# Optimization experiments

Measured on AMD Instinct MI355X. Metric: run time of the kernel, lower is better.

## Reference

```python
import jax, jax.numpy as jnp
import numpy as np

IN_F = 64
EDGE_F = 64
B, N = 2, 512


def setup_inputs() -> dict:
    key = jax.random.key(0)
    ks = jax.random.split(key, 10)
    h = jax.random.normal(ks[0], (B, N, IN_F), dtype=jnp.float32)
    edge = jax.random.normal(ks[1], (B, N, N, EDGE_F), dtype=jnp.float32)
    adj = (jax.random.uniform(ks[2], (B, N, N)) < 0.5).astype(jnp.float32)
    lin_in = 2 * IN_F + EDGE_F
    s_lin = 1.0 / np.sqrt(lin_in)
    s_gru = 1.0 / np.sqrt(EDGE_F)
    W_lin = jax.random.uniform(ks[3], (EDGE_F, lin_in), minval=-s_lin, maxval=s_lin)
    b_lin = jax.random.uniform(ks[4], (EDGE_F,), minval=-s_lin, maxval=s_lin)
    w_ih = jax.random.uniform(ks[5], (3 * EDGE_F, EDGE_F), minval=-s_gru, maxval=s_gru)
    w_hh = jax.random.uniform(ks[6], (3 * EDGE_F, EDGE_F), minval=-s_gru, maxval=s_gru)
    b_ih = jax.random.uniform(ks[7], (3 * EDGE_F,), minval=-s_gru, maxval=s_gru)
    b_hh = jax.random.uniform(ks[8], (3 * EDGE_F,), minval=-s_gru, maxval=s_gru)
    return {"h": h, "edge": edge, "adj": adj, "W_lin": W_lin, "b_lin": b_lin,
            "w_ih": w_ih, "w_hh": w_hh, "b_ih": b_ih, "b_hh": b_hh}


def reference(h, edge, adj, W_lin, b_lin, w_ih, w_hh, b_ih, b_hh):
    F_ = h.shape[-1]
    E = edge.shape[-1]
    # Split the concat-linear: cat = [h1, edge, h2] where h1[b,i,j]=h[b,j], h2[b,i,j]=h[b,i].
    W1 = W_lin[:, :F_]            # cols acting on h1
    We = W_lin[:, F_:F_ + E]      # cols acting on edge
    W2 = W_lin[:, F_ + E:]        # cols acting on h2
    t1 = jnp.einsum('bjf,ef->bje', h, W1)[:, None, :, :]   # broadcast over i
    t2 = jnp.einsum('bif,ef->bie', h, W2)[:, :, None, :]   # broadcast over j
    te = jnp.einsum('bije,fe->bijf', edge, We)
    m = (t1 + te + t2 + b_lin) * adj[..., None]            # [b,N,N,E]
    # GRUCell: input = m, hidden = edge
    gi = jnp.einsum('bije,ge->bijg', m, w_ih) + b_ih        # [b,N,N,3E]
    gh = jnp.einsum('bije,ge->bijg', edge, w_hh) + b_hh
    i_r, i_z, i_n = jnp.split(gi, 3, axis=-1)
    h_r, h_z, h_n = jnp.split(gh, 3, axis=-1)
    r = jax.nn.sigmoid(i_r + h_r)
    z = jax.nn.sigmoid(i_z + h_z)
    n = jnp.tanh(i_n + r * h_n)
    new_h = (1.0 - z) * n + z * edge
    return jax.nn.silu(new_h)
```

## Files before the change

### kernel.cpp

```cpp
#include <hip/hip_runtime.h>
#include <hip/hip_bf16.h>

#define B_ 2
#define N_ 512
#define E_ 64
#define G_ 192
#define LIN_IN_ 192

typedef __attribute__((ext_vector_type(8))) short bf16x8;
typedef __attribute__((ext_vector_type(4))) float f32x4;

__device__ __forceinline__ unsigned short f2bf(float x) {
  unsigned u = __float_as_uint(x);
  unsigned r = (u + 0x7FFFu + ((u >> 16) & 1u)) >> 16;
  return (unsigned short)r;
}
__device__ __forceinline__ float sigm(float x) { return 1.f / (1.f + __expf(-x)); }
__device__ __forceinline__ float tanh_f(float x) {
  float e = __expf(-2.f * fabsf(x));
  return copysignf((1.f - e) / (1.f + e), x);
}
__device__ __forceinline__ bf16x8 pack8(const float* t) {
  union { bf16x8 v; __hip_bfloat16 h[8]; } u;
#pragma unroll
  for (int k = 0; k < 8; ++k) u.h[k] = __float2bfloat16(t[k]);
  return u.v;
}

__global__ __launch_bounds__(64) void prep1(const float* __restrict__ Wlin,
                                            const float* __restrict__ blin,
                                            const float* __restrict__ wih,
                                            const float* __restrict__ whh,
                                            unsigned short* __restrict__ Bt,
                                            float* __restrict__ V1,
                                            float* __restrict__ V2,
                                            float* __restrict__ ub) {
  int g = blockIdx.x;
  int f = threadIdx.x;
  if (g < G_) {
    const float* wr = wih + g * 64;
    float aw = 0.f, a1 = 0.f, a2 = 0.f;
#pragma unroll
    for (int e = 0; e < 64; ++e) {
      float wv = wr[e];
      a1 += wv * Wlin[e * LIN_IN_ + f];
      aw += wv * Wlin[e * LIN_IN_ + 64 + f];
      a2 += wv * Wlin[e * LIN_IN_ + 128 + f];
    }
    Bt[g * 64 + f] = f2bf(aw);
    V1[g * 64 + f] = a1;
    V2[g * 64 + f] = a2;
    if (f == 0) {
      float s = 0.f;
      for (int e = 0; e < 64; ++e) s += wr[e] * blin[e];
      ub[g] = s;
    }
  } else {
    int gh = g - G_;
    Bt[g * 64 + f] = f2bf(whh[gh * 64 + f]);
  }
}

__global__ __launch_bounds__(192) void prep2(const float* __restrict__ h,
                                             const float* __restrict__ V1,
                                             const float* __restrict__ V2,
                                             const float* __restrict__ ub,
                                             float* __restrict__ u1,
                                             float* __restrict__ u2p) {
  int row = blockIdx.x;
  int g = threadIdx.x;
  const float* hr = h + (size_t)row * 64;
  float a1 = 0.f, a2 = 0.f;
#pragma unroll
  for (int f = 0; f < 64; ++f) {
    float hv = hr[f];
    a1 += V1[g * 64 + f] * hv;
    a2 += V2[g * 64 + f] * hv;
  }
  u1[(size_t)row * G_ + g] = a1;
  u2p[(size_t)row * G_ + g] = a2 + ub[g];
}

__global__ __launch_bounds__(256, 3) void fusedT3(const float* __restrict__ edge,
                                                  const float* __restrict__ adj,
                                                  const unsigned short* __restrict__ BtW,
                                                  const float* __restrict__ u1,
                                                  const float* __restrict__ u2p,
                                                  const float* __restrict__ bih,
                                                  const float* __restrict__ bhh,
                                                  float* __restrict__ out) {
  __shared__ uint4 Bs4[3072];
  char* Bc = (char*)Bs4;
  int tid = threadIdx.x;
  const uint4* src = (const uint4*)BtW;
#pragma unroll
  for (int it = 0; it < 12; ++it) {
    int c = tid + it * 256;
    int row = c >> 3;
    *(uint4*)(Bc + row * 128 + (((c & 7) * 16) ^ ((row & 7) << 4))) = src[c];
  }
  __syncthreads();

  int lane = tid & 63, wave = tid >> 6;
  unsigned pbase = blockIdx.x * 128u + wave * 32u;
  int b = pbase >> 18;
  int iN = (pbase >> 9) & 511;
  int j0w = pbase & 511;
  int lr = lane & 15, lg = lane >> 4;

  bf16x8 efrag[2][2];
  float adjv[2];
#pragma unroll
  for (int np = 0; np < 2; ++np) {
    const float* er = edge + (size_t)(pbase + np * 16 + lr) * 64 + lg * 8;
    float tmp[8];
#pragma unroll
    for (int s = 0; s < 2; ++s) {
      *(float4*)tmp = *(const float4*)(er + s * 32);
      *(float4*)(tmp + 4) = *(const float4*)(er + s * 32 + 4);
      efrag[np][s] = pack8(tmp);
    }
    adjv[np] = adj[pbase + np * 16 + lr];
  }

  int addrE = (lr + 16 * (lg >> 1)) << 2;
  int addrO = addrE + 128;

  const float* u2r = u2p + ((size_t)(b * N_ + iN)) * G_;
  const float* u1b = u1 + ((size_t)(b * N_ + j0w)) * G_;

  f32x4 yo[2][4];

#pragma unroll
  for (int mg = 0; mg < 4; ++mg) {
    int e0 = mg * 16 + lg * 4;
    f32x4 acc[2][6];
    f32x4 zero = {0.f, 0.f, 0.f, 0.f};
#pragma unroll
    for (int np = 0; np < 2; ++np)
#pragma unroll
      for (int w = 0; w < 6; ++w) acc[np][w] = zero;

    const int tiles[6] = {mg, mg + 4, mg + 8, mg + 12, mg + 16, mg + 20};
#pragma unroll
    for (int s = 0; s < 2; ++s) {
      bf16x8 wf[6];
#pragma unroll
      for (int w = 0; w < 6; ++w) {
        int R = tiles[w] * 16 + lr;
        wf[w] = *(const bf16x8*)(Bc + R * 128 +
                                 ((s * 64 + lg * 16) ^ ((R & 7) << 4)));
      }
#pragma unroll
      for (int np = 0; np < 2; ++np)
#pragma unroll
        for (int w = 0; w < 6; ++w)
          acc[np][w] = __builtin_amdgcn_mfma_f32_16x16x32_bf16(
              wf[w], efrag[np][s], acc[np][w], 0, 0, 0);
    }

    f32x4 u2v0 = *(const f32x4*)(u2r + e0);
    f32x4 u2v1 = *(const f32x4*)(u2r + 64 + e0);
    f32x4 u2v2 = *(const f32x4*)(u2r + 128 + e0);
    f32x4 bc0 = *(const f32x4*)(bih + e0) + *(const f32x4*)(bhh + e0);
    f32x4 bc1 = *(const f32x4*)(bih + 64 + e0) + *(const f32x4*)(bhh + 64 + e0);
    f32x4 bi2 = *(const f32x4*)(bih + 128 + e0);
    f32x4 bh2 = *(const f32x4*)(bhh + 128 + e0);

#pragma unroll
    for (int np = 0; np < 2; ++np) {
      const float* u1r = u1b + (size_t)(np * 16 + lr) * G_;
      f32x4 u1v0 = *(const f32x4*)(u1r + e0);
      f32x4 u1v1 = *(const f32x4*)(u1r + 64 + e0);
      f32x4 u1v2 = *(const f32x4*)(u1r + 128 + e0);

      union { bf16x8 v; int d[4]; } ef;
      ef.v = efrag[np][mg >> 1];
      int addr = (mg & 1) ? addrO : addrE;
      int r0 = __builtin_amdgcn_ds_bpermute(addr, ef.d[0]);
      int r1 = __builtin_amdgcn_ds_bpermute(addr, ef.d[1]);
      int r2 = __builtin_amdgcn_ds_bpermute(addr, ef.d[2]);
      int r3 = __builtin_amdgcn_ds_bpermute(addr, ef.d[3]);
      bool hi = (lg & 1);
      unsigned w0 = (unsigned)(hi ? r2 : r0);
      unsigned w1 = (unsigned)(hi ? r3 : r1);
      float eva[4];
      eva[0] = __uint_as_float(w0 << 16);
      eva[1] = __uint_as_float(w0 & 0xffff0000u);
      eva[2] = __uint_as_float(w1 << 16);
      eva[3] = __uint_as_float(w1 & 0xffff0000u);

      float a = adjv[np];
      f32x4 yv;
#pragma unroll
      for (int reg = 0; reg < 4; ++reg) {
        float s1 = a * (acc[np][0][reg] + u1v0[reg] + u2v0[reg]) + bc0[reg] +
                   acc[np][3][reg];
        float s2 = a * (acc[np][1][reg] + u1v1[reg] + u2v1[reg]) + bc1[reg] +
                   acc[np][4][reg];
        float gin = a * (acc[np][2][reg] + u1v2[reg] + u2v2[reg]) + bi2[reg];
        float ghn = acc[np][5][reg] + bh2[reg];
        float r = sigm(s1);
        float z = sigm(s2);
        float n = tanh_f(gin + r * ghn);
        float y = (1.f - z) * n + z * eva[reg];
        yv[reg] = y * sigm(y);
      }
      yo[np][mg] = yv;
    }
  }

#pragma unroll
  for (int np = 0; np < 2; ++np) {
    size_t P = pbase + np * 16 + lr;
    float* op = out + P * 64 + lg * 4;
#pragma unroll
    for (int mg = 0; mg < 4; ++mg)
      *(f32x4*)(op + mg * 16) = yo[np][mg];
  }
}

__global__ __launch_bounds__(64) void mkernelF(const float* __restrict__ edge,
                                               const float* __restrict__ adj,
                                               const float* __restrict__ Wlin,
                                               const float* __restrict__ blin,
                                               const float* __restrict__ h,
                                               float* __restrict__ mout) {
  size_t p = (size_t)blockIdx.x * 64 + threadIdx.x;
  int b = (int)(p >> 18), i = (int)((p >> 9) & 511), j = (int)(p & 511);
  float ed[E_], hj[E_], hi[E_];
  const float4* ep = (const float4*)(edge + p * E_);
  const float4* hjp = (const float4*)(h + ((size_t)(b * N_ + j)) * E_);
  const float4* hip = (const float4*)(h + ((size_t)(b * N_ + i)) * E_);
#pragma unroll
  for (int k = 0; k < E_ / 4; ++k) {
    float4 v = ep[k];
    ed[4 * k] = v.x; ed[4 * k + 1] = v.y; ed[4 * k + 2] = v.z; ed[4 * k + 3] = v.w;
    float4 a = hjp[k];
    hj[4 * k] = a.x; hj[4 * k + 1] = a.y; hj[4 * k + 2] = a.z; hj[4 * k + 3] = a.w;
    float4 u = hip[k];
    hi[4 * k] = u.x; hi[4 * k + 1] = u.y; hi[4 * k + 2] = u.z; hi[4 * k + 3] = u.w;
  }
  float av = adj[p];
  float* mo = mout + p * E_;
  for (int e = 0; e < E_; ++e) {
    const float* w = Wlin + e * LIN_IN_;
    float acc = blin[e];
#pragma unroll
    for (int k = 0; k < E_; ++k)
      acc += hj[k] * w[k] + ed[k] * w[64 + k] + hi[k] * w[128 + k];
    mo[e] = av * acc;
  }
}
__global__ __launch_bounds__(64) void gkernelF(const float* __restrict__ edge,
                                               const float* mbuf,
                                               const float* __restrict__ wih,
                                               const float* __restrict__ whh,
                                               const float* __restrict__ bih,
                                               const float* __restrict__ bhh,
                                               float* out) {
  size_t p = (size_t)blockIdx.x * 64 + threadIdx.x;
  float ed[E_], m[E_];
  const float4* ep = (const float4*)(edge + p * E_);
  const float4* mp = (const float4*)(mbuf + p * E_);
#pragma unroll
  for (int k = 0; k < E_ / 4; ++k) {
    float4 v = ep[k];
    ed[4 * k] = v.x; ed[4 * k + 1] = v.y; ed[4 * k + 2] = v.z; ed[4 * k + 3] = v.w;
    float4 u = mp[k];
    m[4 * k] = u.x; m[4 * k + 1] = u.y; m[4 * k + 2] = u.z; m[4 * k + 3] = u.w;
  }
  float* op = out + p * E_;
  for (int e = 0; e < E_; ++e) {
    const float* wr = wih + e * 64;
    const float* wz = wih + (64 + e) * 64;
    const float* wn = wih + (128 + e) * 64;
    const float* vr = whh + e * 64;
    const float* vz = whh + (64 + e) * 64;
    const float* vn = whh + (128 + e) * 64;
    float ir = bih[e], iz = bih[64 + e], inn = bih[128 + e];
    float hr = bhh[e], hz = bhh[64 + e], hn = bhh[128 + e];
#pragma unroll
    for (int k = 0; k < E_; ++k) {
      float mk = m[k], ek = ed[k];
      ir += mk * wr[k]; iz += mk * wz[k]; inn += mk * wn[k];
      hr += ek * vr[k]; hz += ek * vz[k]; hn += ek * vn[k];
    }
    float r = sigm(ir + hr);
    float z = sigm(iz + hz);
    float nv = tanh_f(inn + r * hn);
    float nh = (1.f - z) * nv + z * ed[e];
    op[e] = nh * sigm(nh);
  }
}

extern "C" void kernel_launch(void* const* d_in, const int* in_sizes, int n_in,
                              void* d_out, int out_size, void* d_ws, size_t ws_size,
                              hipStream_t stream) {
  const float* h    = (const float*)d_in[0];
  const float* edge = (const float*)d_in[1];
  const float* adj  = (const float*)d_in[2];
  const float* Wlin = (const float*)d_in[3];
  const float* blin = (const float*)d_in[4];
  const float* wih  = (const float*)d_in[5];
  const float* whh  = (const float*)d_in[6];
  const float* bih  = (const float*)d_in[7];
  const float* bhh  = (const float*)d_in[8];
  float* out = (float*)d_out;

  const size_t OFF_V1 = 49152, OFF_V2 = 98304, OFF_UB = 147456,
               OFF_U1 = 148480, OFF_U2 = 148480 + 786432;
  const size_t WS_NEEDED = OFF_U2 + 786432;
  if (ws_size >= WS_NEEDED) {
    char* w = (char*)d_ws;
    unsigned short* Bt = (unsigned short*)w;
    float* V1 = (float*)(w + OFF_V1);
    float* V2 = (float*)(w + OFF_V2);
    float* ub = (float*)(w + OFF_UB);
    float* u1 = (float*)(w + OFF_U1);
    float* u2p = (float*)(w + OFF_U2);
    prep1<<<384, 64, 0, stream>>>(Wlin, blin, wih, whh, Bt, V1, V2, ub);
    prep2<<<B_ * N_, 192, 0, stream>>>(h, V1, V2, ub, u1, u2p);
    fusedT3<<<(B_ * N_ * N_) / 128, 256, 0, stream>>>(edge, adj, Bt, u1, u2p,
                                                      bih, bhh, out);
  } else {
    size_t npairs = (size_t)B_ * N_ * N_;
    int blocks = (int)(npairs / 64);
    mkernelF<<<blocks, 64, 0, stream>>>(edge, adj, Wlin, blin, h, out);
    gkernelF<<<blocks, 64, 0, stream>>>(edge, out, wih, whh, bih, bhh, out);
  }
}
```

Before: 148.8 us.

## Make fused GRU kernel persistent over four tiles with register prefetch of edges

The grid shrinks from 4096 to 1024 blocks, and each block now processes four 128-pair tiles. This amortizes the per-block staging of weights into LDS across four tiles instead of one. While one tile computes, the edge and adj data for the next tile is prefetched into registers to hide global load latency. tanh is rewritten as 2*sigmoid(2x)-1 and the GRU blend is simplified. The occupancy hint of 3 blocks is dropped, so the extra prefetch registers may lower occupancy.

```diff
diff --git a/kernel.cpp b/kernel.cpp
--- a/kernel.cpp
+++ b/kernel.cpp
@@ -81,14 +81,14 @@
   u2p[(size_t)row * G_ + g] = a2 + ub[g];
 }
 
-__global__ __launch_bounds__(256, 3) void fusedT3(const float* __restrict__ edge,
-                                                  const float* __restrict__ adj,
-                                                  const unsigned short* __restrict__ BtW,
-                                                  const float* __restrict__ u1,
-                                                  const float* __restrict__ u2p,
-                                                  const float* __restrict__ bih,
-                                                  const float* __restrict__ bhh,
-                                                  float* __restrict__ out) {
+__global__ __launch_bounds__(256) void fusedT7(const float* __restrict__ edge,
+                                               const float* __restrict__ adj,
+                                               const unsigned short* __restrict__ BtW,
+                                               const float* __restrict__ u1,
+                                               const float* __restrict__ u2p,
+                                               const float* __restrict__ bih,
+                                               const float* __restrict__ bhh,
+                                               float* __restrict__ out) {
   __shared__ uint4 Bs4[3072];
   char* Bc = (char*)Bs4;
   int tid = threadIdx.x;
@@ -103,120 +103,151 @@
 
   int lane = tid & 63, wave = tid >> 6;
   unsigned pbase = blockIdx.x * 128u + wave * 32u;
-  int b = pbase >> 18;
-  int iN = (pbase >> 9) & 511;
-  int j0w = pbase & 511;
   int lr = lane & 15, lg = lane >> 4;
 
-  bf16x8 efrag[2][2];
-  float adjv[2];
+  int addrE = (lr + 16 * (lg >> 1)) << 2;
+  int addrO = addrE + 128;
+
+  float4 raw[2][4];
+  float adjraw[2];
+
 #pragma unroll
   for (int np = 0; np < 2; ++np) {
     const float* er = edge + (size_t)(pbase + np * 16 + lr) * 64 + lg * 8;
-    float tmp[8];
-#pragma unroll
-    for (int s = 0; s < 2; ++s) {
-      *(float4*)tmp = *(const float4*)(er + s * 32);
-      *(float4*)(tmp + 4) = *(const float4*)(er + s * 32 + 4);
-      efrag[np][s] = pack8(tmp);
-    }
-    adjv[np] = adj[pbase + np * 16 + lr];
-  }
-
-  int addrE = (lr + 16 * (lg >> 1)) << 2;
-  int addrO = addrE + 128;
-
-  const float* u2r = u2p + ((size_t)(b * N_ + iN)) * G_;
-  const float* u1b = u1 + ((size_t)(b * N_ + j0w)) * G_;
-
-  f32x4 yo[2][4];
-
-#pragma unroll
-  for (int mg = 0; mg < 4; ++mg) {
-    int e0 = mg * 16 + lg * 4;
-    f32x4 acc[2][6];
-    f32x4 zero = {0.f, 0.f, 0.f, 0.f};
-#pragma unroll
-    for (int np = 0; np < 2; ++np)
-#pragma unroll
-      for (int w = 0; w < 6; ++w) acc[np][w] = zero;
-
-    const int tiles[6] = {mg, mg + 4, mg + 8, mg + 12, mg + 16, mg + 20};
-#pragma unroll
-    for (int s = 0; s < 2; ++s) {
-      bf16x8 wf[6];
-#pragma unroll
-      for (int w = 0; w < 6; ++w) {
-        int R = tiles[w] * 16 + lr;
-        wf[w] = *(const bf16x8*)(Bc + R * 128 +
-                                 ((s * 64 + lg * 16) ^ ((R & 7) << 4)));
+    raw[np][0] = *(const float4*)er;
+    raw[np][1] = *(const float4*)(er + 4);
+    raw[np][2] = *(const float4*)(er + 32);
+    raw[np][3] = *(const float4*)(er + 36);
+    adjraw[np] = adj[pbase + np * 16 + lr];
+  }
+
+#pragma unroll
+  for (int t = 0; t < 4; ++t) {
+    unsigned ptile = pbase + (unsigned)t * 131072u;
+    int b = ptile >> 18;
+    int iN = (ptile >> 9) & 511;
+    int j0w = ptile & 511;
+
+    bf16x8 efrag[2][2];
+    float adjv[2];
+#pragma unroll
+    for (int np = 0; np < 2; ++np) {
+#pragma unroll
+      for (int s = 0; s < 2; ++s) {
+        float tmp[8];
+        *(float4*)tmp = raw[np][s * 2];
+        *(float4*)(tmp + 4) = raw[np][s * 2 + 1];
+        efrag[np][s] = pack8(tmp);
       }
+      adjv[np] = adjraw[np];
+    }
+
+    if (t < 3) {
+      unsigned pnext = pbase + (unsigned)(t + 1) * 131072u;
+#pragma unroll
+      for (int np = 0; np < 2; ++np) {
+        const float* er = edge + (size_t)(pnext + np * 16 + lr) * 64 + lg * 8;
+        raw[np][0] = *(const float4*)er;
+        raw[np][1] = *(const float4*)(er + 4);
+        raw[np][2] = *(const float4*)(er + 32);
+        raw[np][3] = *(const float4*)(er + 36);
+        adjraw[np] = adj[pnext + np * 16 + lr];
+      }
+    }
+
+    const float* u2r = u2p + ((size_t)(b * N_ + iN)) * G_;
+    const float* u1b = u1 + ((size_t)(b * N_ + j0w)) * G_;
+
+    f32x4 yo[2][4];
+
+#pragma unroll
+    for (int mg = 0; mg < 4; ++mg) {
+      int e0 = mg * 16 + lg * 4;
+      f32x4 acc[2][6];
+      f32x4 zero = {0.f, 0.f, 0.f, 0.f};
 #pragma unroll
       for (int np = 0; np < 2; ++np)
 #pragma unroll
-        for (int w = 0; w < 6; ++w)
-          acc[np][w] = __builtin_amdgcn_mfma_f32_16x16x32_bf16(
-              wf[w], efrag[np][s], acc[np][w], 0, 0, 0);
-    }
-
-    f32x4 u2v0 = *(const f32x4*)(u2r + e0);
-    f32x4 u2v1 = *(const f32x4*)(u2r + 64 + e0);
-    f32x4 u2v2 = *(const f32x4*)(u2r + 128 + e0);
-    f32x4 bc0 = *(const f32x4*)(bih + e0) + *(const f32x4*)(bhh + e0);
-    f32x4 bc1 = *(const f32x4*)(bih + 64 + e0) + *(const f32x4*)(bhh + 64 + e0);
-    f32x4 bi2 = *(const f32x4*)(bih + 128 + e0);
-    f32x4 bh2 = *(const f32x4*)(bhh + 128 + e0);
+        for (int w = 0; w < 6; ++w) acc[np][w] = zero;
+
+      const int tiles[6] = {mg, mg + 4, mg + 8, mg + 12, mg + 16, mg + 20};
+#pragma unroll
+      for (int s = 0; s < 2; ++s) {
+        bf16x8 wf[6];
+#pragma unroll
+        for (int w = 0; w < 6; ++w) {
+          int R = tiles[w] * 16 + lr;
+          wf[w] = *(const bf16x8*)(Bc + R * 128 +
+                                   ((s * 64 + lg * 16) ^ ((R & 7) << 4)));
+        }
+#pragma unroll
+        for (int np = 0; np < 2; ++np)
+#pragma unroll
+          for (int w = 0; w < 6; ++w)
+            acc[np][w] = __builtin_amdgcn_mfma_f32_16x16x32_bf16(
+                wf[w], efrag[np][s], acc[np][w], 0, 0, 0);
+      }
+
+      f32x4 u2v0 = *(const f32x4*)(u2r + e0);
+      f32x4 u2v1 = *(const f32x4*)(u2r + 64 + e0);
+      f32x4 u2v2 = *(const f32x4*)(u2r + 128 + e0);
+      f32x4 bc0 = *(const f32x4*)(bih + e0) + *(const f32x4*)(bhh + e0);
+      f32x4 bc1 = *(const f32x4*)(bih + 64 + e0) + *(const f32x4*)(bhh + 64 + e0);
+      f32x4 bi2 = *(const f32x4*)(bih + 128 + e0);
+      f32x4 bh2 = *(const f32x4*)(bhh + 128 + e0);
+
+#pragma unroll
+      for (int np = 0; np < 2; ++np) {
+        const float* u1r = u1b + (size_t)(np * 16 + lr) * G_;
+        f32x4 u1v0 = *(const f32x4*)(u1r + e0);
+        f32x4 u1v1 = *(const f32x4*)(u1r + 64 + e0);
+        f32x4 u1v2 = *(const f32x4*)(u1r + 128 + e0);
+
+        union { bf16x8 v; int d[4]; } ef;
+        ef.v = efrag[np][mg >> 1];
+        int addr = (mg & 1) ? addrO : addrE;
+        int r0 = __builtin_amdgcn_ds_bpermute(addr, ef.d[0]);
+        int r1 = __builtin_amdgcn_ds_bpermute(addr, ef.d[1]);
+        int r2 = __builtin_amdgcn_ds_bpermute(addr, ef.d[2]);
+        int r3 = __builtin_amdgcn_ds_bpermute(addr, ef.d[3]);
+        bool hi = (lg & 1);
+        unsigned w0 = (unsigned)(hi ? r2 : r0);
+        unsigned w1 = (unsigned)(hi ? r3 : r1);
+        float eva[4];
+        eva[0] = __uint_as_float(w0 << 16);
+        eva[1] = __uint_as_float(w0 & 0xffff0000u);
+        eva[2] = __uint_as_float(w1 << 16);
+        eva[3] = __uint_as_float(w1 & 0xffff0000u);
+
+        float a = adjv[np];
+        f32x4 yv;
+#pragma unroll
+        for (int reg = 0; reg < 4; ++reg) {
+          float s1 = a * (acc[np][0][reg] + u1v0[reg] + u2v0[reg]) + bc0[reg] +
+                     acc[np][3][reg];
+          float s2 = a * (acc[np][1][reg] + u1v1[reg] + u2v1[reg]) + bc1[reg] +
+                     acc[np][4][reg];
+          float gin = a * (acc[np][2][reg] + u1v2[reg] + u2v2[reg]) + bi2[reg];
+          float ghn = acc[np][5][reg] + bh2[reg];
+          float r = sigm(s1);
+          float z = sigm(s2);
+          float tt = gin + r * ghn;
+          float n = 2.f * sigm(2.f * tt) - 1.f;
+          float y = n + z * (eva[reg] - n);
+          yv[reg] = y * sigm(y);
+        }
+        yo[np][mg] = yv;
+      }
+    }
 
 #pragma unroll
     for (int np = 0; np < 2; ++np) {
-      const float* u1r = u1b + (size_t)(np * 16 + lr) * G_;
-      f32x4 u1v0 = *(const f32x4*)(u1r + e0);
-      f32x4 u1v1 = *(const f32x4*)(u1r + 64 + e0);
-      f32x4 u1v2 = *(const f32x4*)(u1r + 128 + e0);
-
-      union { bf16x8 v; int d[4]; } ef;
-      ef.v = efrag[np][mg >> 1];
-      int addr = (mg & 1) ? addrO : addrE;
-      int r0 = __builtin_amdgcn_ds_bpermute(addr, ef.d[0]);
-      int r1 = __builtin_amdgcn_ds_bpermute(addr, ef.d[1]);
-      int r2 = __builtin_amdgcn_ds_bpermute(addr, ef.d[2]);
-      int r3 = __builtin_amdgcn_ds_bpermute(addr, ef.d[3]);
-      bool hi = (lg & 1);
-      unsigned w0 = (unsigned)(hi ? r2 : r0);
-      unsigned w1 = (unsigned)(hi ? r3 : r1);
-      float eva[4];
-      eva[0] = __uint_as_float(w0 << 16);
-      eva[1] = __uint_as_float(w0 & 0xffff0000u);
-      eva[2] = __uint_as_float(w1 << 16);
-      eva[3] = __uint_as_float(w1 & 0xffff0000u);
-
-      float a = adjv[np];
-      f32x4 yv;
-#pragma unroll
-      for (int reg = 0; reg < 4; ++reg) {
-        float s1 = a * (acc[np][0][reg] + u1v0[reg] + u2v0[reg]) + bc0[reg] +
-                   acc[np][3][reg];
-        float s2 = a * (acc[np][1][reg] + u1v1[reg] + u2v1[reg]) + bc1[reg] +
-                   acc[np][4][reg];
-        float gin = a * (acc[np][2][reg] + u1v2[reg] + u2v2[reg]) + bi2[reg];
-        float ghn = acc[np][5][reg] + bh2[reg];
-        float r = sigm(s1);
-        float z = sigm(s2);
-        float n = tanh_f(gin + r * ghn);
-        float y = (1.f - z) * n + z * eva[reg];
-        yv[reg] = y * sigm(y);
-      }
-      yo[np][mg] = yv;
-    }
-  }
-
-#pragma unroll
-  for (int np = 0; np < 2; ++np) {
-    size_t P = pbase + np * 16 + lr;
-    float* op = out + P * 64 + lg * 4;
-#pragma unroll
-    for (int mg = 0; mg < 4; ++mg)
-      *(f32x4*)(op + mg * 16) = yo[np][mg];
+      size_t P = ptile + np * 16 + lr;
+      float* op = out + P * 64 + lg * 4;
+#pragma unroll
+      for (int mg = 0; mg < 4; ++mg)
+        *(f32x4*)(op + mg * 16) = yo[np][mg];
+    }
   }
 }
 
@@ -321,8 +352,7 @@
     float* u2p = (float*)(w + OFF_U2);
     prep1<<<384, 64, 0, stream>>>(Wlin, blin, wih, whh, Bt, V1, V2, ub);
     prep2<<<B_ * N_, 192, 0, stream>>>(h, V1, V2, ub, u1, u2p);
-    fusedT3<<<(B_ * N_ * N_) / 128, 256, 0, stream>>>(edge, adj, Bt, u1, u2p,
-                                                      bih, bhh, out);
+    fusedT7<<<1024, 256, 0, stream>>>(edge, adj, Bt, u1, u2p, bih, bhh, out);
   } else {
     size_t npairs = (size_t)B_ * N_ * N_;
     int blocks = (int)(npairs / 64);
```

Result: slower. 199.0 us (+33.8%).
